# Kernel tuning notes

Measured on AMD Instinct MI355X. Metric: run time of the kernel, lower is better.

Reference implementation:

```python
import jax, jax.numpy as jnp
import numpy as np

N = 200000          # total instances
NUM_BAGS = 25000    # ragged bags, avg size 8
D = 690             # repre_size
R = 53              # rel_size


def setup_inputs() -> dict:
    key = jax.random.key(0)
    k1, k2, k3 = jax.random.split(key, 3)
    repre = jax.random.normal(k1, (N, D), dtype=jnp.float32)
    relation_mat = jax.random.normal(k2, (R, D), dtype=jnp.float32) * 0.001
    bias = jnp.zeros((R,), dtype=jnp.float32)
    labels = jax.random.randint(k3, (N,), 0, R, dtype=jnp.int64)
    # ragged contiguous scopes partitioning [0, N)
    rng = np.random.default_rng(0)
    cuts = np.sort(rng.choice(np.arange(1, N), size=NUM_BAGS - 1, replace=False))
    starts = np.concatenate([[0], cuts])
    ends = np.concatenate([cuts, [N]])
    scope = jnp.asarray(np.stack([starts, ends], axis=1), dtype=jnp.int64)
    return {"repre": repre, "relation_mat": relation_mat, "bias": bias,
            "scope": scope, "labels": labels}


def reference(repre, relation_mat, bias, scope, labels):
    # training / use_bag path of AttentionSelector.forward
    starts = scope[:, 0]
    # segment id for each instance (scopes are a contiguous partition)
    seg = jnp.searchsorted(starts, jnp.arange(N), side="right") - 1  # [N]
    rel_vecs = relation_mat[labels]                      # [N, D]
    rel_logits = jnp.sum(repre * rel_vecs, axis=-1)      # [N]
    # segment softmax (numerically stable)
    m = jax.ops.segment_max(rel_logits, seg, num_segments=NUM_BAGS)
    e = jnp.exp(rel_logits - m[seg])
    denom = jax.ops.segment_sum(e, seg, num_segments=NUM_BAGS)
    w = e / denom[seg]                                   # [N]
    att_repres = jax.ops.segment_sum(w[:, None] * repre, seg,
                                     num_segments=NUM_BAGS)  # [NUM_BAGS, D]
    logits = att_repres @ relation_mat.T + bias          # [NUM_BAGS, R]
    return logits
```

## Files before the change

### kernel.cpp

```cpp
#include <hip/hip_runtime.h>


#define NBAGS_TOT 25000
#define DDIM      690
#define D2        345
#define RREL      53
#define G_BAGS    8
#define MAXBAG    1024
#define BLOCK     256

__global__ __launch_bounds__(BLOCK) void bag_attn_kernel(
    const float* __restrict__ repre,
    const float* __restrict__ rel,
    const float* __restrict__ bias,
    const int*   __restrict__ scope,
    const int*   __restrict__ labels,
    float*       __restrict__ out)
{
    __shared__ float s_w[MAXBAG];
    __shared__ float s_att[G_BAGS * DDIM];
    __shared__ float s_red[8];

    const int tid  = threadIdx.x;
    const int lane = tid & 63;
    const int wave = tid >> 6;
    const int bag0 = blockIdx.x * G_BAGS;

    const float2* rel2 = (const float2*)rel;

    for (int g = 0; g < G_BAGS; ++g) {
        const int bag   = bag0 + g;
        const int start = scope[2 * bag];
        const int end   = scope[2 * bag + 1];
        int size = end - start;
        if (size > MAXBAG) size = MAXBAG;

        for (int j = wave; j < size; j += 4) {
            const int row = start + j;
            const float2* rp = (const float2*)(repre + (size_t)row * DDIM);
            const float2* rl = rel2 + (size_t)labels[row] * D2;
            float acc = 0.f;
            #pragma unroll
            for (int k = 0; k < 6; ++k) {
                int f = lane + 64 * k;
                if (f < D2) {
                    float2 v = rp[f];
                    float2 u = rl[f];
                    acc = fmaf(v.x, u.x, fmaf(v.y, u.y, acc));
                }
            }
            #pragma unroll
            for (int o = 32; o; o >>= 1) acc += __shfl_xor(acc, o, 64);
            if (lane == 0) s_w[j] = acc;
        }
        __syncthreads();

        float lm = -3.402823466e38f;
        for (int j = tid; j < size; j += BLOCK) lm = fmaxf(lm, s_w[j]);
        #pragma unroll
        for (int o = 32; o; o >>= 1) lm = fmaxf(lm, __shfl_xor(lm, o, 64));
        if (lane == 0) s_red[wave] = lm;
        __syncthreads();
        const float m = fmaxf(fmaxf(s_red[0], s_red[1]),
                              fmaxf(s_red[2], s_red[3]));
        __syncthreads();

        float ls = 0.f;
        for (int j = tid; j < size; j += BLOCK) {
            float e = expf(s_w[j] - m);
            s_w[j] = e;
            ls += e;
        }
        #pragma unroll
        for (int o = 32; o; o >>= 1) ls += __shfl_xor(ls, o, 64);
        if (lane == 0) s_red[wave] = ls;
        __syncthreads();
        const float inv = 1.f / (s_red[0] + s_red[1] + s_red[2] + s_red[3]);
        for (int j = tid; j < size; j += BLOCK) s_w[j] *= inv;
        __syncthreads();

        float2* att2 = (float2*)(s_att + g * DDIM);
        for (int f = tid; f < D2; f += BLOCK) {
            float ax = 0.f, ay = 0.f;
            const float2* rp = (const float2*)(repre + (size_t)start * DDIM) + f;
            for (int j = 0; j < size; ++j) {
                const float w  = s_w[j];
                const float2 v = rp[(size_t)j * D2];
                ax = fmaf(w, v.x, ax);
                ay = fmaf(w, v.y, ay);
            }
            att2[f] = make_float2(ax, ay);
        }
        __syncthreads();
    }

    for (int r = wave; r < RREL; r += 4) {
        const float2* rl = rel2 + (size_t)r * D2;
        float acc[G_BAGS];
        #pragma unroll
        for (int g = 0; g < G_BAGS; ++g) acc[g] = 0.f;
        #pragma unroll
        for (int k = 0; k < 6; ++k) {
            int f = lane + 64 * k;
            if (f < D2) {
                float2 u = rl[f];
                #pragma unroll
                for (int g = 0; g < G_BAGS; ++g) {
                    const float2* a2 = (const float2*)(s_att + g * DDIM);
                    float2 a = a2[f];
                    acc[g] = fmaf(u.x, a.x, fmaf(u.y, a.y, acc[g]));
                }
            }
        }
        const float b = bias[r];
        #pragma unroll
        for (int g = 0; g < G_BAGS; ++g) {
            float v = acc[g];
            #pragma unroll
            for (int o = 32; o; o >>= 1) v += __shfl_xor(v, o, 64);
            if (lane == 0) out[(size_t)(bag0 + g) * RREL + r] = v + b;
        }
    }
}

extern "C" void kernel_launch(void* const* d_in, const int* in_sizes, int n_in,
                              void* d_out, int out_size, void* d_ws, size_t ws_size,
                              hipStream_t stream)
{
    const float* repre  = (const float*)d_in[0];
    const float* rel    = (const float*)d_in[1];
    const float* bias   = (const float*)d_in[2];
    const int*   scope  = (const int*)d_in[3];
    const int*   labels = (const int*)d_in[4];
    float*       out    = (float*)d_out;

    const int grid = NBAGS_TOT / G_BAGS;
    bag_attn_kernel<<<grid, BLOCK, 0, stream>>>(repre, rel, bias, scope, labels, out);
}
```

Baseline: 1.043 ms.

## Use one wave per bag with online softmax single-pass accumulation

```diff
diff --git a/kernel.cpp b/kernel.cpp
--- a/kernel.cpp
+++ b/kernel.cpp
@@ -1,15 +1,14 @@
 #include <hip/hip_runtime.h>
 
 
-#define NBAGS_TOT 25000
-#define DDIM      690
-#define D2        345
-#define RREL      53
-#define G_BAGS    8
-#define MAXBAG    1024
-#define BLOCK     256
+#define NBAGS  25000
+#define DDIM   690
+#define D2     345
+#define RREL   53
+#define WAVES  8
+#define BLOCK  512
 
-__global__ __launch_bounds__(BLOCK) void bag_attn_kernel(
+__global__ __launch_bounds__(BLOCK, 4) void bag_attn_kernel(
     const float* __restrict__ repre,
     const float* __restrict__ rel,
     const float* __restrict__ bias,
@@ -17,108 +16,90 @@
     const int*   __restrict__ labels,
     float*       __restrict__ out)
 {
-    __shared__ float s_w[MAXBAG];
-    __shared__ float s_att[G_BAGS * DDIM];
-    __shared__ float s_red[8];
+    __shared__ float s_att[WAVES * DDIM];
 
     const int tid  = threadIdx.x;
     const int lane = tid & 63;
     const int wave = tid >> 6;
-    const int bag0 = blockIdx.x * G_BAGS;
+    const int bag  = blockIdx.x * WAVES + wave;
+
+    const int start = scope[2 * bag];
+    const int end   = scope[2 * bag + 1];
 
     const float2* rel2 = (const float2*)rel;
 
-    for (int g = 0; g < G_BAGS; ++g) {
-        const int bag   = bag0 + g;
-        const int start = scope[2 * bag];
-        const int end   = scope[2 * bag + 1];
-        int size = end - start;
-        if (size > MAXBAG) size = MAXBAG;
+    float2 acc[6];
+    #pragma unroll
+    for (int k = 0; k < 6; ++k) acc[k] = make_float2(0.f, 0.f);
+    float m = -3.402823466e38f;
+    float l = 0.f;
 
-        for (int j = wave; j < size; j += 4) {
-            const int row = start + j;
-            const float2* rp = (const float2*)(repre + (size_t)row * DDIM);
-            const float2* rl = rel2 + (size_t)labels[row] * D2;
-            float acc = 0.f;
+    for (int row = start; row < end; ++row) {
+        const float2* rp = (const float2*)(repre + (size_t)row * DDIM);
+        const float2* rl = rel2 + (size_t)labels[row] * D2;
+
+        float2 v[6];
+        float dot = 0.f;
+        #pragma unroll
+        for (int k = 0; k < 6; ++k) {
+            const int f = lane + 64 * k;
+            if (f < D2) {
+                v[k] = rp[f];
+                const float2 u = rl[f];
+                dot = fmaf(v[k].x, u.x, fmaf(v[k].y, u.y, dot));
+            } else {
+                v[k] = make_float2(0.f, 0.f);
+            }
+        }
+        #pragma unroll
+        for (int o = 32; o; o >>= 1) dot += __shfl_xor(dot, o, 64);
+
+        const float nm = fmaxf(m, dot);
+        const float sc = __expf(m - nm);
+        const float e  = __expf(dot - nm);
+        l = fmaf(l, sc, e);
+        #pragma unroll
+        for (int k = 0; k < 6; ++k) {
+            acc[k].x = fmaf(acc[k].x, sc, e * v[k].x);
+            acc[k].y = fmaf(acc[k].y, sc, e * v[k].y);
+        }
+        m = nm;
+    }
+
+    const float inv = 1.f / l;
+    float2* satt2 = (float2*)(s_att + wave * DDIM);
+    #pragma unroll
+    for (int k = 0; k < 6; ++k) {
+        const int f = lane + 64 * k;
+        if (f < D2) satt2[f] = make_float2(acc[k].x * inv, acc[k].y * inv);
+    }
+    __syncthreads();
+
+    const int bag0 = blockIdx.x * WAVES;
+    for (int r = wave; r < RREL; r += WAVES) {
+        const float2* rl = rel2 + (size_t)r * D2;
+        float2 u[6];
+        #pragma unroll
+        for (int k = 0; k < 6; ++k) {
+            const int f = lane + 64 * k;
+            u[k] = (f < D2) ? rl[f] : make_float2(0.f, 0.f);
+        }
+        const float b = bias[r];
+        #pragma unroll
+        for (int g = 0; g < WAVES; ++g) {
+            const float2* a2 = (const float2*)(s_att + g * DDIM);
+            float dot = 0.f;
             #pragma unroll
             for (int k = 0; k < 6; ++k) {
-                int f = lane + 64 * k;
+                const int f = lane + 64 * k;
                 if (f < D2) {
-                    float2 v = rp[f];
-                    float2 u = rl[f];
-                    acc = fmaf(v.x, u.x, fmaf(v.y, u.y, acc));
+                    const float2 a = a2[f];
+                    dot = fmaf(u[k].x, a.x, fmaf(u[k].y, a.y, dot));
                 }
             }
             #pragma unroll
-            for (int o = 32; o; o >>= 1) acc += __shfl_xor(acc, o, 64);
-            if (lane == 0) s_w[j] = acc;
-        }
-        __syncthreads();
-
-        float lm = -3.402823466e38f;
-        for (int j = tid; j < size; j += BLOCK) lm = fmaxf(lm, s_w[j]);
-        #pragma unroll
-        for (int o = 32; o; o >>= 1) lm = fmaxf(lm, __shfl_xor(lm, o, 64));
-        if (lane == 0) s_red[wave] = lm;
-        __syncthreads();
-        const float m = fmaxf(fmaxf(s_red[0], s_red[1]),
-                              fmaxf(s_red[2], s_red[3]));
-        __syncthreads();
-
-        float ls = 0.f;
-        for (int j = tid; j < size; j += BLOCK) {
-            float e = expf(s_w[j] - m);
-            s_w[j] = e;
-            ls += e;
-        }
-        #pragma unroll
-        for (int o = 32; o; o >>= 1) ls += __shfl_xor(ls, o, 64);
-        if (lane == 0) s_red[wave] = ls;
-        __syncthreads();
-        const float inv = 1.f / (s_red[0] + s_red[1] + s_red[2] + s_red[3]);
-        for (int j = tid; j < size; j += BLOCK) s_w[j] *= inv;
-        __syncthreads();
-
-        float2* att2 = (float2*)(s_att + g * DDIM);
-        for (int f = tid; f < D2; f += BLOCK) {
-            float ax = 0.f, ay = 0.f;
-            const float2* rp = (const float2*)(repre + (size_t)start * DDIM) + f;
-            for (int j = 0; j < size; ++j) {
-                const float w  = s_w[j];
-                const float2 v = rp[(size_t)j * D2];
-                ax = fmaf(w, v.x, ax);
-                ay = fmaf(w, v.y, ay);
-            }
-            att2[f] = make_float2(ax, ay);
-        }
-        __syncthreads();
-    }
-
-    for (int r = wave; r < RREL; r += 4) {
-        const float2* rl = rel2 + (size_t)r * D2;
-        float acc[G_BAGS];
-        #pragma unroll
-        for (int g = 0; g < G_BAGS; ++g) acc[g] = 0.f;
-        #pragma unroll
-        for (int k = 0; k < 6; ++k) {
-            int f = lane + 64 * k;
-            if (f < D2) {
-                float2 u = rl[f];
-                #pragma unroll
-                for (int g = 0; g < G_BAGS; ++g) {
-                    const float2* a2 = (const float2*)(s_att + g * DDIM);
-                    float2 a = a2[f];
-                    acc[g] = fmaf(u.x, a.x, fmaf(u.y, a.y, acc[g]));
-                }
-            }
-        }
-        const float b = bias[r];
-        #pragma unroll
-        for (int g = 0; g < G_BAGS; ++g) {
-            float v = acc[g];
-            #pragma unroll
-            for (int o = 32; o; o >>= 1) v += __shfl_xor(v, o, 64);
-            if (lane == 0) out[(size_t)(bag0 + g) * RREL + r] = v + b;
+            for (int o = 32; o; o >>= 1) dot += __shfl_xor(dot, o, 64);
+            if (lane == 0) out[(size_t)(bag0 + g) * RREL + r] = dot + b;
         }
     }
 }
@@ -134,6 +115,6 @@
     const int*   labels = (const int*)d_in[4];
     float*       out    = (float*)d_out;
 
-    const int grid = NBAGS_TOT / G_BAGS;
+    const int grid = NBAGS / WAVES;
     bag_attn_kernel<<<grid, BLOCK, 0, stream>>>(repre, rel, bias, scope, labels, out);
 }
```

Result: faster. 994.5 us (-4.7%).
